# Kernel optimization log

Measured on AMD Instinct MI355X. Metric: run time of the kernel, lower is better.

The kernel has to match this reference:

```python
import jax, jax.numpy as jnp
import numpy as np

B, T, D, R = 8, 4096, 1024, 1024
INIT = 0.02

def setup_inputs() -> dict:
    key = jax.random.key(0)
    ks = jax.random.split(key, 8)
    x = jax.random.normal(ks[0], (B, T, D), dtype=jnp.float32)
    attention_mask = jnp.ones((B, T), dtype=bool)
    W_Q = jax.random.normal(ks[1], (D, D), dtype=jnp.float32) * (1.0 / np.sqrt(D))
    W_K = jax.random.normal(ks[2], (D, D), dtype=jnp.float32) * (1.0 / np.sqrt(D))
    U = jax.random.normal(ks[3], (D, R), dtype=jnp.float32) * INIT
    V = jax.random.normal(ks[4], (D, R), dtype=jnp.float32) * INIT
    Wb = jax.random.normal(ks[5], (D, R), dtype=jnp.float32) * INIT
    bias = jnp.zeros((D,), dtype=jnp.float32)
    W_O = jax.random.normal(ks[6], (D, D), dtype=jnp.float32) * (1.0 / np.sqrt(D))
    return {"x": x, "attention_mask": attention_mask, "W_Q": W_Q, "W_K": W_K,
            "U": U, "V": V, "Wb": Wb, "bias": bias, "W_O": W_O}

def reference(x, attention_mask, W_Q, W_K, U, V, Wb, bias, W_O):
    # Q = x @ W_Q^T, K = x @ W_K^T  (torch Linear stores weight as (out,in))
    Q = jnp.einsum('btd,ed->bte', x, W_Q)
    K = jnp.einsum('btd,ed->bte', x, W_K)
    m = attention_mask.astype(x.dtype)               # (B,T)
    A = Q @ V                                        # (B,T,R)  = Q_i V
    Kw = (K @ Wb) * m[..., None]                     # pad-masked K_j W
    S = jnp.cumsum(Kw, axis=1)                       # causal prefix sum over j<=i
    n = jnp.cumsum(m, axis=1)[..., None]             # n_valid per i, (B,T,1)
    # sum_{j<=i} BCN(Q_i,K_j) = ((Q_iV) * S_i) U^T + n_i * bias; then divide by max(n_i,1)
    out = ((A * S) @ U.T + n * bias) / jnp.clip(n, 1.0)
    return jnp.einsum('btd,ed->bte', out, W_O)
```

## Files before the change

kernel.cpp:

```cpp
#include <hip/hip_runtime.h>
#include <hip/hip_bf16.h>

typedef __attribute__((ext_vector_type(8))) short short8;
typedef __attribute__((ext_vector_type(4))) float f32x4;

#define Bc 8
#define Tc 4096
#define Dc 1024
#define Rc 1024
#define BT (Bc*Tc)

__device__ inline float b2f(ushort u) {
    union { float f; unsigned int i; } x; x.i = ((unsigned int)u) << 16; return x.f;
}
__device__ inline ushort f2b(float f) {
    union { float f; unsigned int i; } x; x.f = f;
    unsigned int r = x.i + 0x7fffu + ((x.i >> 16) & 1u);
    return (ushort)(r >> 16);
}

__device__ inline void gload16(const void* g, void* l) {
    __builtin_amdgcn_global_load_lds(
        (const __attribute__((address_space(1))) unsigned int*)g,
        (__attribute__((address_space(3))) unsigned int*)l, 16, 0, 0);
}


__device__ __attribute__((always_inline)) inline
short8 lds_frag(const char* mat, int rowbase, int k, int fr, int hi) {
    const int row = rowbase + fr;
    const int byte = (row << 7) + (((k << 6) + (hi << 4)) ^ ((row & 7) << 4));
    return *(const short8*)(mat + byte);
}

template<int KK>
__device__ __attribute__((always_inline)) inline
void rdb(const char* BB, short8 (&bf)[2][4], int wn, int fr, int hi) {
#pragma unroll
    for (int n = 0; n < 4; ++n)
        bf[KK][n] = lds_frag(BB, (wn << 6) + (n << 4), KK, fr, hi);
}

template<int MQ, int KK>
__device__ __attribute__((always_inline)) inline
void rda(const char* AB, short8 (&af)[4], int wm, int fr, int hi) {
#pragma unroll
    for (int i = 0; i < 4; ++i)
        af[i] = lds_frag(AB, (wm << 7) + ((MQ * 4 + i) << 4), KK, fr, hi);
}

template<int MQ, int KK>
__device__ __attribute__((always_inline)) inline
void mmq(f32x4 (&acc)[8][4], const short8 (&af)[4], const short8 (&bf)[2][4]) {
#pragma unroll
    for (int i = 0; i < 4; ++i)
#pragma unroll
        for (int n = 0; n < 4; ++n)
            acc[MQ * 4 + i][n] = __builtin_amdgcn_mfma_f32_16x16x32_bf16(
                af[i], bf[KK][n], acc[MQ * 4 + i][n], 0, 0, 0);
}

#define MID do { __builtin_amdgcn_sched_barrier(0); __builtin_amdgcn_s_barrier(); \
    asm volatile("s_waitcnt lgkmcnt(0)" ::: "memory"); __builtin_amdgcn_sched_barrier(0); \
    __builtin_amdgcn_s_setprio(1); } while (0)
#define PEND do { __builtin_amdgcn_s_setprio(0); __builtin_amdgcn_sched_barrier(0); \
    __builtin_amdgcn_s_barrier(); } while (0)
#define PENDVM do { __builtin_amdgcn_s_setprio(0); __builtin_amdgcn_sched_barrier(0); \
    asm volatile("s_waitcnt vmcnt(4)" ::: "memory"); __builtin_amdgcn_s_barrier(); } while (0)

#define STG(G, ld, grow0, gk, lbase) do { \
    const ushort* _s0 = (G) + (size_t)((grow0) + srow) * (ld) + (gk) + scg; \
    const ushort* _s1 = (G) + (size_t)((grow0) + 64 + srow) * (ld) + (gk) + scg; \
    char* _d = (lbase) + (w << 10) + (l << 4); \
    gload16(_s0, _d); gload16(_s1, _d + 8192); } while (0)

template<int EPI>
__global__ __launch_bounds__(512, 2)
void gemm256(const ushort* __restrict__ A, const ushort* __restrict__ Bt,
             void* __restrict__ Cout, const float* __restrict__ bias,
             int ntx, int K, int lda, int ldb, int ldc) {
    __shared__ __align__(16) char sA[65536];
    __shared__ __align__(16) char sB[65536];

    const int tid = threadIdx.x;
    const int w = tid >> 6, l = tid & 63;
    const int wm = w >> 2, wn = w & 3;
    const int fr = l & 15, hi = l >> 4;
    const int srow = (w << 3) + (l >> 3);
    const int scg = (((l & 7) ^ (l >> 3)) << 3);

    const int nwg = (int)gridDim.x;
    const int q = nwg >> 3;
    const int bid = (int)blockIdx.x;
    const int swz = (bid & 7) * q + (bid >> 3);
    const int by = swz / ntx, bx = swz % ntx;
    const int m0 = by << 8, n0 = bx << 8;

    f32x4 acc[8][4] = {};
    short8 af[4], bf[2][4];
    const int NT = K >> 6;

    STG(A,  lda, m0,        0,  sA);
    STG(A,  lda, m0 + 128,  0,  sA + 16384);
    STG(Bt, ldb, n0,        0,  sB);
    STG(Bt, ldb, n0 + 128,  0,  sB + 16384);
    STG(Bt, ldb, n0,        64, sB + 32768);
    STG(Bt, ldb, n0 + 128,  64, sB + 32768 + 16384);
    asm volatile("s_waitcnt vmcnt(4)" ::: "memory");
    __builtin_amdgcn_sched_barrier(0);
    __builtin_amdgcn_s_barrier();

    const char* cA0 = sA;
    const char* cB0 = sB;
    const char* cA1 = sA + 32768;
    const char* cB1 = sB + 32768;

    for (int it = 0; it < (NT >> 1); ++it) {
        const int t1 = 2 * it + 1;
        const int t2 = min(2 * it + 2, NT - 1);
        const int t3 = min(2 * it + 3, NT - 1);

        rdb<0>(cB0, bf, wn, fr, hi); rdb<1>(cB0, bf, wn, fr, hi);
        rda<0, 0>(cA0, af, wm, fr, hi);
        STG(A, lda, m0, t1 << 6, sA + 32768);
        MID; mmq<0, 0>(acc, af, bf); PEND;
        rda<1, 0>(cA0, af, wm, fr, hi);
        STG(A, lda, m0 + 128, t1 << 6, sA + 32768 + 16384);
        MID; mmq<1, 0>(acc, af, bf); PEND;
        rda<0, 1>(cA0, af, wm, fr, hi);
        STG(Bt, ldb, n0, t2 << 6, sB);
        MID; mmq<0, 1>(acc, af, bf); PEND;
        rda<1, 1>(cA0, af, wm, fr, hi);
        STG(Bt, ldb, n0 + 128, t2 << 6, sB + 16384);
        MID; mmq<1, 1>(acc, af, bf); PENDVM;

        rdb<0>(cB1, bf, wn, fr, hi); rdb<1>(cB1, bf, wn, fr, hi);
        rda<0, 0>(cA1, af, wm, fr, hi);
        STG(A, lda, m0, t2 << 6, sA);
        MID; mmq<0, 0>(acc, af, bf); PEND;
        rda<1, 0>(cA1, af, wm, fr, hi);
        STG(A, lda, m0 + 128, t2 << 6, sA + 16384);
        MID; mmq<1, 0>(acc, af, bf); PEND;
        rda<0, 1>(cA1, af, wm, fr, hi);
        STG(Bt, ldb, n0, t3 << 6, sB + 32768);
        MID; mmq<0, 1>(acc, af, bf); PEND;
        rda<1, 1>(cA1, af, wm, fr, hi);
        STG(Bt, ldb, n0 + 128, t3 << 6, sB + 32768 + 16384);
        MID; mmq<1, 1>(acc, af, bf); PENDVM;
    }

    const int crow = m0 + (wm << 7);
    const int ccol = n0 + (wn << 6);
#pragma unroll
    for (int m = 0; m < 8; ++m) {
#pragma unroll
        for (int n = 0; n < 4; ++n) {
            const int r0 = crow + (m << 4) + (hi << 2);
            const int c = ccol + (n << 4) + fr;
            if (EPI == 0) {
                ushort* C = (ushort*)Cout;
#pragma unroll
                for (int t = 0; t < 4; ++t)
                    C[(size_t)(r0 + t) * ldc + c] = f2b(acc[m][n][t]);
            } else {
                float* C = (float*)Cout;
                const float bv = bias[c];
#pragma unroll
                for (int t = 0; t < 4; ++t)
                    C[(size_t)(r0 + t) * ldc + c] = acc[m][n][t] + bv;
            }
        }
    }
}

__global__ void cast_f32_bf16(const float4* __restrict__ in, ushort4* __restrict__ out, int n4) {
    int i = blockIdx.x * blockDim.x + threadIdx.x;
    int stride = gridDim.x * blockDim.x;
    for (; i < n4; i += stride) {
        float4 v = in[i];
        ushort4 o;
        o.x = f2b(v.x); o.y = f2b(v.y); o.z = f2b(v.z); o.w = f2b(v.w);
        out[i] = o;
    }
}

__global__ void transpose_cast(const float* __restrict__ in, ushort* __restrict__ out,
                               int rows, int cols) {
    __shared__ float tile[32][33];
    int c0 = blockIdx.x * 32, r0 = blockIdx.y * 32;
    int tx = threadIdx.x & 31, ty = threadIdx.x >> 5;
    for (int i = 0; i < 32; i += 8)
        tile[ty + i][tx] = in[(size_t)(r0 + ty + i) * cols + c0 + tx];
    __syncthreads();
    for (int i = 0; i < 32; i += 8)
        out[(size_t)(c0 + ty + i) * rows + r0 + tx] = f2b(tile[tx][ty + i]);
}

__global__ __launch_bounds__(256)
void gemm_bt_kernel(const ushort* __restrict__ A, const ushort* __restrict__ Bt,
                    ushort* __restrict__ Cout,
                    int M, int N, int K, int lda, int ldb, int ldc) {
    __shared__ __align__(16) ushort As[128][32];
    __shared__ __align__(16) ushort Bs[128][32];
    const int tid = threadIdx.x;
    const int wave = tid >> 6, lane = tid & 63;
    const int m0 = blockIdx.y * 128, n0 = blockIdx.x * 128;
    const int wr = (wave >> 1) * 64, wc = (wave & 1) * 64;

    f32x4 acc[4][4] = {};

    const int rS = wave * 32 + (lane >> 2);
    const int kS = (lane & 3) * 8;
    const int fr = lane & 15;
    const int fq = (lane >> 4) * 8;

    const int nk = K >> 5;
    for (int kt = 0; kt < nk; ++kt) {
        const int k0 = kt << 5;
        __syncthreads();
        gload16(A  + (size_t)(m0 + rS) * lda      + k0 + kS, &As[rS][kS]);
        gload16(A  + (size_t)(m0 + rS + 16) * lda + k0 + kS, &As[rS + 16][kS]);
        gload16(Bt + (size_t)(n0 + rS) * ldb      + k0 + kS, &Bs[rS][kS]);
        gload16(Bt + (size_t)(n0 + rS + 16) * ldb + k0 + kS, &Bs[rS + 16][kS]);
        __syncthreads();

        short8 af[4], bfr[4];
        #pragma unroll
        for (int i = 0; i < 4; i++) af[i]  = *(const short8*)&As[wr + i * 16 + fr][fq];
        #pragma unroll
        for (int i = 0; i < 4; i++) bfr[i] = *(const short8*)&Bs[wc + i * 16 + fr][fq];
        #pragma unroll
        for (int i = 0; i < 4; i++)
            #pragma unroll
            for (int j = 0; j < 4; j++)
                acc[i][j] = __builtin_amdgcn_mfma_f32_16x16x32_bf16(af[i], bfr[j], acc[i][j], 0, 0, 0);
    }

    const int rq = (lane >> 4) * 4;
    #pragma unroll
    for (int i = 0; i < 4; i++) {
        #pragma unroll
        for (int j = 0; j < 4; j++) {
            int row = m0 + wr + i * 16 + rq;
            int col = n0 + wc + j * 16 + fr;
            #pragma unroll
            for (int t = 0; t < 4; t++)
                Cout[(size_t)(row + t) * ldc + col] = f2b(acc[i][j][t]);
        }
    }
}

__global__ void bias_O_kernel(const float* __restrict__ W_O, const float* __restrict__ bias,
                              float* __restrict__ biasO) {
    __shared__ float sh[256];
    int e = blockIdx.x, tid = threadIdx.x;
    float s = 0.f;
    for (int d = tid; d < Dc; d += 256) s += W_O[(size_t)e * Dc + d] * bias[d];
    sh[tid] = s; __syncthreads();
    for (int o = 128; o > 0; o >>= 1) { if (tid < o) sh[tid] += sh[tid + o]; __syncthreads(); }
    if (tid == 0) biasO[e] = sh[0];
}

__global__ void mask_scan(const int* __restrict__ mask, float* __restrict__ nbuf) {
    __shared__ float sh[256];
    int b = blockIdx.x, tid = threadIdx.x;
    float run = 0.f;
    for (int t0 = 0; t0 < Tc; t0 += 256) {
        float v = (mask[b * Tc + t0 + tid] != 0) ? 1.f : 0.f;
        sh[tid] = v; __syncthreads();
        for (int off = 1; off < 256; off <<= 1) {
            float add = (tid >= off) ? sh[tid - off] : 0.f;
            __syncthreads();
            sh[tid] += add;
            __syncthreads();
        }
        nbuf[b * Tc + t0 + tid] = run + sh[tid];
        run += sh[255];
        __syncthreads();
    }
}

#define NCHUNK 16
#define LCHUNK (Tc / NCHUNK)

__global__ void scan_partial(const ushort* __restrict__ AKw, const int* __restrict__ mask,
                             float* __restrict__ csum) {
    int r = blockIdx.x * 256 + threadIdx.x;
    int chunk = blockIdx.y, b = blockIdx.z;
    int row0 = b * Tc + chunk * LCHUNK;
    const ushort* p = AKw + (size_t)row0 * 2048 + 1024 + r;
    float s = 0.f;
    for (int t = 0; t < LCHUNK; ++t) {
        float mv = (mask[row0 + t] != 0) ? 1.f : 0.f;
        s += mv * b2f(p[(size_t)t * 2048]);
    }
    csum[((size_t)b * NCHUNK + chunk) * Rc + r] = s;
}

__global__ void scan_offsets(float* __restrict__ csum) {
    int r = blockIdx.x * 256 + threadIdx.x;
    int b = blockIdx.y;
    float run = 0.f;
    for (int c = 0; c < NCHUNK; ++c) {
        size_t i = ((size_t)b * NCHUNK + c) * Rc + r;
        float v = csum[i]; csum[i] = run; run += v;
    }
}

__global__ void scan_apply(ushort* __restrict__ AKw, const int* __restrict__ mask,
                           const float* __restrict__ csum, const float* __restrict__ nbuf) {
    int r = blockIdx.x * 256 + threadIdx.x;
    int chunk = blockIdx.y, b = blockIdx.z;
    int row0 = b * Tc + chunk * LCHUNK;
    float s = csum[((size_t)b * NCHUNK + chunk) * Rc + r];
    ushort* p = AKw + (size_t)row0 * 2048;
    for (int t = 0; t < LCHUNK; ++t) {
        size_t off = (size_t)t * 2048;
        float mv = (mask[row0 + t] != 0) ? 1.f : 0.f;
        s += mv * b2f(p[off + 1024 + r]);
        float nv = fmaxf(nbuf[row0 + t], 1.f);
        float pv = b2f(p[off + r]) * s / nv;
        p[off + r] = f2b(pv);
    }
}

extern "C" void kernel_launch(void* const* d_in, const int* in_sizes, int n_in,
                              void* d_out, int out_size, void* d_ws, size_t ws_size,
                              hipStream_t stream) {
    const float* x    = (const float*)d_in[0];
    const int*   mask = (const int*)d_in[1];
    const float* W_Q  = (const float*)d_in[2];
    const float* W_K  = (const float*)d_in[3];
    const float* U    = (const float*)d_in[4];
    const float* V    = (const float*)d_in[5];
    const float* Wb   = (const float*)d_in[6];
    const float* bias = (const float*)d_in[7];
    const float* W_O  = (const float*)d_in[8];
    float* out = (float*)d_out;

    char* ws = (char*)d_ws;
    ushort* xb   = (ushort*)ws; ws += (size_t)BT * Dc * 2;
    ushort* AKw  = (ushort*)ws; ws += (size_t)BT * 2048 * 2;
    ushort* W1   = (ushort*)ws; ws += (size_t)2048 * Dc * 2;
    ushort* Mmat = (ushort*)ws; ws += (size_t)Dc * Rc * 2;
    ushort* Vt   = (ushort*)ws; ws += (size_t)Dc * Rc * 2;
    ushort* Wbt  = (ushort*)ws; ws += (size_t)Dc * Rc * 2;
    ushort* Ut   = (ushort*)ws; ws += (size_t)Dc * Rc * 2;
    ushort* WQt  = (ushort*)ws; ws += (size_t)Dc * Dc * 2;
    ushort* WKt  = (ushort*)ws; ws += (size_t)Dc * Dc * 2;
    ushort* WOb  = (ushort*)ws; ws += (size_t)Dc * Dc * 2;
    float*  csum = (float*)ws;  ws += (size_t)Bc * NCHUNK * Rc * 4;
    float*  nbuf = (float*)ws;  ws += (size_t)Bc * Tc * 4;
    float*  biasO = (float*)ws; ws += (size_t)Dc * 4;

    cast_f32_bf16<<<2048, 256, 0, stream>>>((const float4*)x, (ushort4*)xb, BT * Dc / 4);
    cast_f32_bf16<<<256, 256, 0, stream>>>((const float4*)W_O, (ushort4*)WOb, Dc * Dc / 4);

    transpose_cast<<<dim3(32, 32), 256, 0, stream>>>(V,   Vt,  Dc, Rc);
    transpose_cast<<<dim3(32, 32), 256, 0, stream>>>(Wb,  Wbt, Dc, Rc);
    transpose_cast<<<dim3(32, 32), 256, 0, stream>>>(U,   Ut,  Dc, Rc);
    transpose_cast<<<dim3(32, 32), 256, 0, stream>>>(W_Q, WQt, Dc, Dc);
    transpose_cast<<<dim3(32, 32), 256, 0, stream>>>(W_K, WKt, Dc, Dc);

    gemm_bt_kernel<<<dim3(8, 8), 256, 0, stream>>>(Vt,  WQt, W1,                   Rc, Dc, Dc, Dc, Dc, Dc);
    gemm_bt_kernel<<<dim3(8, 8), 256, 0, stream>>>(Wbt, WKt, W1 + (size_t)Rc * Dc, Rc, Dc, Dc, Dc, Dc, Dc);
    gemm_bt_kernel<<<dim3(8, 8), 256, 0, stream>>>(WOb, Ut,  Mmat,                 Dc, Rc, Dc, Dc, Dc, Rc);
    bias_O_kernel<<<Dc, 256, 0, stream>>>(W_O, bias, biasO);

    gemm256<0><<<1024, 512, 0, stream>>>(xb, W1, AKw, nullptr, 8, Dc, Dc, Dc, 2048);

    mask_scan<<<Bc, 256, 0, stream>>>(mask, nbuf);
    scan_partial<<<dim3(4, NCHUNK, Bc), 256, 0, stream>>>(AKw, mask, csum);
    scan_offsets<<<dim3(4, Bc), 256, 0, stream>>>(csum);
    scan_apply<<<dim3(4, NCHUNK, Bc), 256, 0, stream>>>(AKw, mask, csum, nbuf);

    gemm256<1><<<512, 512, 0, stream>>>(AKw, Mmat, out, biasO, 4, Rc, 2048, Rc, Dc);
}
```

Measured before the change: 452.7 us.

## Restructure GEMM pipeline, batch weight prep kernels, vectorize chunked scan

Reworks the main GEMM inner loop so each 64-wide K step double-buffers A fragments, drops the per-phase lgkmcnt(0) wait, and precomputes per-thread global and LDS offsets. Merges the five transpose-casts plus the W_O cast into one launch, and the three small weight GEMMs into one z-batched launch. Rewrites the scan kernels to use 64 chunks, have each thread handle four columns with vector loads, skip masked rows, and multiply by a reciprocal instead of dividing. Removing the lgkmcnt wait leans on the compiler to insert its own LDS waits, and the extra fragment registers could hurt occupancy.

```diff
diff --git a/kernel.cpp b/kernel.cpp
--- a/kernel.cpp
+++ b/kernel.cpp
@@ -60,19 +60,38 @@
                 af[i], bf[KK][n], acc[MQ * 4 + i][n], 0, 0, 0);
 }
 
-#define MID do { __builtin_amdgcn_sched_barrier(0); __builtin_amdgcn_s_barrier(); \
-    asm volatile("s_waitcnt lgkmcnt(0)" ::: "memory"); __builtin_amdgcn_sched_barrier(0); \
+#define PH_MID do { __builtin_amdgcn_sched_barrier(0); __builtin_amdgcn_s_barrier(); \
     __builtin_amdgcn_s_setprio(1); } while (0)
-#define PEND do { __builtin_amdgcn_s_setprio(0); __builtin_amdgcn_sched_barrier(0); \
+#define PH_END do { __builtin_amdgcn_s_setprio(0); __builtin_amdgcn_sched_barrier(0); \
     __builtin_amdgcn_s_barrier(); } while (0)
-#define PENDVM do { __builtin_amdgcn_s_setprio(0); __builtin_amdgcn_sched_barrier(0); \
-    asm volatile("s_waitcnt vmcnt(4)" ::: "memory"); __builtin_amdgcn_s_barrier(); } while (0)
-
-#define STG(G, ld, grow0, gk, lbase) do { \
-    const ushort* _s0 = (G) + (size_t)((grow0) + srow) * (ld) + (gk) + scg; \
-    const ushort* _s1 = (G) + (size_t)((grow0) + 64 + srow) * (ld) + (gk) + scg; \
-    char* _d = (lbase) + (w << 10) + (l << 4); \
-    gload16(_s0, _d); gload16(_s1, _d + 8192); } while (0)
+
+#define STG(G, ld, thr, grow0, gk, lbase) do { \
+    const ushort* _p = (G) + (size_t)(grow0) * (ld) + (gk); \
+    gload16(_p + (thr), (lbase) + thrD); \
+    gload16(_p + (size_t)64 * (ld) + (thr), (lbase) + thrD + 8192); } while (0)
+
+#define TILE(cAb, cBb, stA, stB, tn, tn2) do { \
+     \
+    rdb<0>(cBb, bf, wn, fr, hi); \
+    rda<0, 0>(cAb, afA, wm, fr, hi); \
+    rda<1, 0>(cAb, afB, wm, fr, hi); \
+    STG(A, lda, thrA, m0, (tn) << 6, stA); \
+    PH_MID; mmq<0, 0>(acc, afA, bf); PH_END; \
+     \
+    rdb<1>(cBb, bf, wn, fr, hi); \
+    rda<0, 1>(cAb, afA, wm, fr, hi); \
+    STG(A, lda, thrA, m0 + 128, (tn) << 6, stA + 16384); \
+    PH_MID; mmq<1, 0>(acc, afB, bf); PH_END; \
+     \
+    rda<1, 1>(cAb, afB, wm, fr, hi); \
+    PH_MID; mmq<0, 1>(acc, afA, bf); PH_END; \
+     \
+    STG(Bt, ldb, thrB, n0,       (tn2) << 6, stB); \
+    STG(Bt, ldb, thrB, n0 + 128, (tn2) << 6, stB + 16384); \
+    PH_MID; mmq<1, 1>(acc, afB, bf); \
+    __builtin_amdgcn_s_setprio(0); __builtin_amdgcn_sched_barrier(0); \
+    asm volatile("s_waitcnt vmcnt(4)" ::: "memory"); \
+    __builtin_amdgcn_s_barrier(); } while (0)
 
 template<int EPI>
 __global__ __launch_bounds__(512, 2)
@@ -88,6 +107,9 @@
     const int fr = l & 15, hi = l >> 4;
     const int srow = (w << 3) + (l >> 3);
     const int scg = (((l & 7) ^ (l >> 3)) << 3);
+    const size_t thrA = (size_t)srow * lda + scg;
+    const size_t thrB = (size_t)srow * ldb + scg;
+    const int thrD = (w << 10) + (l << 4);
 
     const int nwg = (int)gridDim.x;
     const int q = nwg >> 3;
@@ -97,15 +119,15 @@
     const int m0 = by << 8, n0 = bx << 8;
 
     f32x4 acc[8][4] = {};
-    short8 af[4], bf[2][4];
+    short8 afA[4], afB[4], bf[2][4];
     const int NT = K >> 6;
 
-    STG(A,  lda, m0,        0,  sA);
-    STG(A,  lda, m0 + 128,  0,  sA + 16384);
-    STG(Bt, ldb, n0,        0,  sB);
-    STG(Bt, ldb, n0 + 128,  0,  sB + 16384);
-    STG(Bt, ldb, n0,        64, sB + 32768);
-    STG(Bt, ldb, n0 + 128,  64, sB + 32768 + 16384);
+    STG(A,  lda, thrA, m0,        0,  sA);
+    STG(A,  lda, thrA, m0 + 128,  0,  sA + 16384);
+    STG(Bt, ldb, thrB, n0,        0,  sB);
+    STG(Bt, ldb, thrB, n0 + 128,  0,  sB + 16384);
+    STG(Bt, ldb, thrB, n0,        64, sB + 32768);
+    STG(Bt, ldb, thrB, n0 + 128,  64, sB + 32768 + 16384);
     asm volatile("s_waitcnt vmcnt(4)" ::: "memory");
     __builtin_amdgcn_sched_barrier(0);
     __builtin_amdgcn_s_barrier();
@@ -119,34 +141,8 @@
         const int t1 = 2 * it + 1;
         const int t2 = min(2 * it + 2, NT - 1);
         const int t3 = min(2 * it + 3, NT - 1);
-
-        rdb<0>(cB0, bf, wn, fr, hi); rdb<1>(cB0, bf, wn, fr, hi);
-        rda<0, 0>(cA0, af, wm, fr, hi);
-        STG(A, lda, m0, t1 << 6, sA + 32768);
-        MID; mmq<0, 0>(acc, af, bf); PEND;
-        rda<1, 0>(cA0, af, wm, fr, hi);
-        STG(A, lda, m0 + 128, t1 << 6, sA + 32768 + 16384);
-        MID; mmq<1, 0>(acc, af, bf); PEND;
-        rda<0, 1>(cA0, af, wm, fr, hi);
-        STG(Bt, ldb, n0, t2 << 6, sB);
-        MID; mmq<0, 1>(acc, af, bf); PEND;
-        rda<1, 1>(cA0, af, wm, fr, hi);
-        STG(Bt, ldb, n0 + 128, t2 << 6, sB + 16384);
-        MID; mmq<1, 1>(acc, af, bf); PENDVM;
-
-        rdb<0>(cB1, bf, wn, fr, hi); rdb<1>(cB1, bf, wn, fr, hi);
-        rda<0, 0>(cA1, af, wm, fr, hi);
-        STG(A, lda, m0, t2 << 6, sA);
-        MID; mmq<0, 0>(acc, af, bf); PEND;
-        rda<1, 0>(cA1, af, wm, fr, hi);
-        STG(A, lda, m0 + 128, t2 << 6, sA + 16384);
-        MID; mmq<1, 0>(acc, af, bf); PEND;
-        rda<0, 1>(cA1, af, wm, fr, hi);
-        STG(Bt, ldb, n0, t3 << 6, sB + 32768);
-        MID; mmq<0, 1>(acc, af, bf); PEND;
-        rda<1, 1>(cA1, af, wm, fr, hi);
-        STG(Bt, ldb, n0 + 128, t3 << 6, sB + 32768 + 16384);
-        MID; mmq<1, 1>(acc, af, bf); PENDVM;
+        TILE(cA0, cB0, sA + 32768, sB, t1, t2);
+        TILE(cA1, cB1, sA, sB + 32768, t2, t3);
     }
 
     const int crow = m0 + (wm << 7);
@@ -184,22 +180,48 @@
     }
 }
 
-__global__ void transpose_cast(const float* __restrict__ in, ushort* __restrict__ out,
-                               int rows, int cols) {
+__global__ void prep_weights(const float* __restrict__ V,  const float* __restrict__ Wb,
+                             const float* __restrict__ U,  const float* __restrict__ WQ,
+                             const float* __restrict__ WK, const float* __restrict__ WO,
+                             ushort* __restrict__ Vt,  ushort* __restrict__ Wbt,
+                             ushort* __restrict__ Ut,  ushort* __restrict__ WQt,
+                             ushort* __restrict__ WKt, ushort* __restrict__ WOb) {
     __shared__ float tile[32][33];
+    const float* in; ushort* out;
+    switch (blockIdx.z) {
+        case 0: in = V;  out = Vt;  break;
+        case 1: in = Wb; out = Wbt; break;
+        case 2: in = U;  out = Ut;  break;
+        case 3: in = WQ; out = WQt; break;
+        case 4: in = WK; out = WKt; break;
+        default: in = WO; out = WOb; break;
+    }
     int c0 = blockIdx.x * 32, r0 = blockIdx.y * 32;
     int tx = threadIdx.x & 31, ty = threadIdx.x >> 5;
-    for (int i = 0; i < 32; i += 8)
-        tile[ty + i][tx] = in[(size_t)(r0 + ty + i) * cols + c0 + tx];
-    __syncthreads();
-    for (int i = 0; i < 32; i += 8)
-        out[(size_t)(c0 + ty + i) * rows + r0 + tx] = f2b(tile[tx][ty + i]);
+    if (blockIdx.z < 5) {
+        for (int i = 0; i < 32; i += 8)
+            tile[ty + i][tx] = in[(size_t)(r0 + ty + i) * 1024 + c0 + tx];
+        __syncthreads();
+        for (int i = 0; i < 32; i += 8)
+            out[(size_t)(c0 + ty + i) * 1024 + r0 + tx] = f2b(tile[tx][ty + i]);
+    } else {
+        for (int i = 0; i < 32; i += 8)
+            out[(size_t)(r0 + ty + i) * 1024 + c0 + tx] =
+                f2b(in[(size_t)(r0 + ty + i) * 1024 + c0 + tx]);
+    }
 }
 
 __global__ __launch_bounds__(256)
-void gemm_bt_kernel(const ushort* __restrict__ A, const ushort* __restrict__ Bt,
-                    ushort* __restrict__ Cout,
-                    int M, int N, int K, int lda, int ldb, int ldc) {
+void gemm_bt3(const ushort* __restrict__ Vt,  const ushort* __restrict__ WQt,
+              const ushort* __restrict__ Wbt, const ushort* __restrict__ WKt,
+              const ushort* __restrict__ WOb, const ushort* __restrict__ Ut,
+              ushort* __restrict__ W1, ushort* __restrict__ Mmat) {
+    const ushort *A, *Bt; ushort* Cout;
+    switch (blockIdx.z) {
+        case 0: A = Vt;  Bt = WQt; Cout = W1; break;
+        case 1: A = Wbt; Bt = WKt; Cout = W1 + (size_t)Rc * Dc; break;
+        default: A = WOb; Bt = Ut; Cout = Mmat; break;
+    }
     __shared__ __align__(16) ushort As[128][32];
     __shared__ __align__(16) ushort Bs[128][32];
     const int tid = threadIdx.x;
@@ -214,14 +236,13 @@
     const int fr = lane & 15;
     const int fq = (lane >> 4) * 8;
 
-    const int nk = K >> 5;
-    for (int kt = 0; kt < nk; ++kt) {
+    for (int kt = 0; kt < 32; ++kt) {
         const int k0 = kt << 5;
         __syncthreads();
-        gload16(A  + (size_t)(m0 + rS) * lda      + k0 + kS, &As[rS][kS]);
-        gload16(A  + (size_t)(m0 + rS + 16) * lda + k0 + kS, &As[rS + 16][kS]);
-        gload16(Bt + (size_t)(n0 + rS) * ldb      + k0 + kS, &Bs[rS][kS]);
-        gload16(Bt + (size_t)(n0 + rS + 16) * ldb + k0 + kS, &Bs[rS + 16][kS]);
+        gload16(A  + (size_t)(m0 + rS) * 1024      + k0 + kS, &As[rS][kS]);
+        gload16(A  + (size_t)(m0 + rS + 16) * 1024 + k0 + kS, &As[rS + 16][kS]);
+        gload16(Bt + (size_t)(n0 + rS) * 1024      + k0 + kS, &Bs[rS][kS]);
+        gload16(Bt + (size_t)(n0 + rS + 16) * 1024 + k0 + kS, &Bs[rS + 16][kS]);
         __syncthreads();
 
         short8 af[4], bfr[4];
@@ -245,7 +266,7 @@
             int col = n0 + wc + j * 16 + fr;
             #pragma unroll
             for (int t = 0; t < 4; t++)
-                Cout[(size_t)(row + t) * ldc + col] = f2b(acc[i][j][t]);
+                Cout[(size_t)(row + t) * 1024 + col] = f2b(acc[i][j][t]);
         }
     }
 }
@@ -280,47 +301,57 @@
     }
 }
 
-#define NCHUNK 16
+#define NCHUNK 64
 #define LCHUNK (Tc / NCHUNK)
 
 __global__ void scan_partial(const ushort* __restrict__ AKw, const int* __restrict__ mask,
                              float* __restrict__ csum) {
-    int r = blockIdx.x * 256 + threadIdx.x;
-    int chunk = blockIdx.y, b = blockIdx.z;
-    int row0 = b * Tc + chunk * LCHUNK;
+    const int r = threadIdx.x * 4;
+    const int chunk = blockIdx.x, b = blockIdx.y;
+    const int row0 = b * Tc + chunk * LCHUNK;
     const ushort* p = AKw + (size_t)row0 * 2048 + 1024 + r;
-    float s = 0.f;
+    float4 s = {0.f, 0.f, 0.f, 0.f};
     for (int t = 0; t < LCHUNK; ++t) {
-        float mv = (mask[row0 + t] != 0) ? 1.f : 0.f;
-        s += mv * b2f(p[(size_t)t * 2048]);
-    }
-    csum[((size_t)b * NCHUNK + chunk) * Rc + r] = s;
+        if (mask[row0 + t] != 0) {
+            ushort4 q = *(const ushort4*)(p + (size_t)t * 2048);
+            s.x += b2f(q.x); s.y += b2f(q.y); s.z += b2f(q.z); s.w += b2f(q.w);
+        }
+    }
+    *(float4*)(csum + (((size_t)b * NCHUNK + chunk) << 10) + r) = s;
 }
 
 __global__ void scan_offsets(float* __restrict__ csum) {
-    int r = blockIdx.x * 256 + threadIdx.x;
-    int b = blockIdx.y;
-    float run = 0.f;
+    const int r = threadIdx.x * 4;
+    const int b = blockIdx.x;
+    float4 run = {0.f, 0.f, 0.f, 0.f};
     for (int c = 0; c < NCHUNK; ++c) {
-        size_t i = ((size_t)b * NCHUNK + c) * Rc + r;
-        float v = csum[i]; csum[i] = run; run += v;
+        float4* p = (float4*)(csum + (((size_t)b * NCHUNK + c) << 10) + r);
+        float4 v = *p; *p = run;
+        run.x += v.x; run.y += v.y; run.z += v.z; run.w += v.w;
     }
 }
 
 __global__ void scan_apply(ushort* __restrict__ AKw, const int* __restrict__ mask,
                            const float* __restrict__ csum, const float* __restrict__ nbuf) {
-    int r = blockIdx.x * 256 + threadIdx.x;
-    int chunk = blockIdx.y, b = blockIdx.z;
-    int row0 = b * Tc + chunk * LCHUNK;
-    float s = csum[((size_t)b * NCHUNK + chunk) * Rc + r];
-    ushort* p = AKw + (size_t)row0 * 2048;
+    const int r = threadIdx.x * 4;
+    const int chunk = blockIdx.x, b = blockIdx.y;
+    const int row0 = b * Tc + chunk * LCHUNK;
+    float4 s = *(const float4*)(csum + (((size_t)b * NCHUNK + chunk) << 10) + r);
+    ushort* p = AKw + (size_t)row0 * 2048 + r;
     for (int t = 0; t < LCHUNK; ++t) {
-        size_t off = (size_t)t * 2048;
-        float mv = (mask[row0 + t] != 0) ? 1.f : 0.f;
-        s += mv * b2f(p[off + 1024 + r]);
-        float nv = fmaxf(nbuf[row0 + t], 1.f);
-        float pv = b2f(p[off + r]) * s / nv;
-        p[off + r] = f2b(pv);
+        const size_t off = (size_t)t * 2048;
+        if (mask[row0 + t] != 0) {
+            ushort4 kw = *(const ushort4*)(p + off + 1024);
+            s.x += b2f(kw.x); s.y += b2f(kw.y); s.z += b2f(kw.z); s.w += b2f(kw.w);
+        }
+        const float rn = 1.f / fmaxf(nbuf[row0 + t], 1.f);
+        ushort4 a = *(const ushort4*)(p + off);
+        ushort4 o;
+        o.x = f2b(b2f(a.x) * s.x * rn);
+        o.y = f2b(b2f(a.y) * s.y * rn);
+        o.z = f2b(b2f(a.z) * s.z * rn);
+        o.w = f2b(b2f(a.w) * s.w * rn);
+        *(ushort4*)(p + off) = o;
     }
 }
 
@@ -354,25 +385,18 @@
     float*  biasO = (float*)ws; ws += (size_t)Dc * 4;
 
     cast_f32_bf16<<<2048, 256, 0, stream>>>((const float4*)x, (ushort4*)xb, BT * Dc / 4);
-    cast_f32_bf16<<<256, 256, 0, stream>>>((const float4*)W_O, (ushort4*)WOb, Dc * Dc / 4);
-
-    transpose_cast<<<dim3(32, 32), 256, 0, stream>>>(V,   Vt,  Dc, Rc);
-    transpose_cast<<<dim3(32, 32), 256, 0, stream>>>(Wb,  Wbt, Dc, Rc);
-    transpose_cast<<<dim3(32, 32), 256, 0, stream>>>(U,   Ut,  Dc, Rc);
-    transpose_cast<<<dim3(32, 32), 256, 0, stream>>>(W_Q, WQt, Dc, Dc);
-    transpose_cast<<<dim3(32, 32), 256, 0, stream>>>(W_K, WKt, Dc, Dc);
-
-    gemm_bt_kernel<<<dim3(8, 8), 256, 0, stream>>>(Vt,  WQt, W1,                   Rc, Dc, Dc, Dc, Dc, Dc);
-    gemm_bt_kernel<<<dim3(8, 8), 256, 0, stream>>>(Wbt, WKt, W1 + (size_t)Rc * Dc, Rc, Dc, Dc, Dc, Dc, Dc);
-    gemm_bt_kernel<<<dim3(8, 8), 256, 0, stream>>>(WOb, Ut,  Mmat,                 Dc, Rc, Dc, Dc, Dc, Rc);
+    prep_weights<<<dim3(32, 32, 6), 256, 0, stream>>>(V, Wb, U, W_Q, W_K, W_O,
+                                                      Vt, Wbt, Ut, WQt, WKt, WOb);
+
+    gemm_bt3<<<dim3(8, 8, 3), 256, 0, stream>>>(Vt, WQt, Wbt, WKt, WOb, Ut, W1, Mmat);
     bias_O_kernel<<<Dc, 256, 0, stream>>>(W_O, bias, biasO);
 
     gemm256<0><<<1024, 512, 0, stream>>>(xb, W1, AKw, nullptr, 8, Dc, Dc, Dc, 2048);
 
     mask_scan<<<Bc, 256, 0, stream>>>(mask, nbuf);
-    scan_partial<<<dim3(4, NCHUNK, Bc), 256, 0, stream>>>(AKw, mask, csum);
-    scan_offsets<<<dim3(4, Bc), 256, 0, stream>>>(csum);
-    scan_apply<<<dim3(4, NCHUNK, Bc), 256, 0, stream>>>(AKw, mask, csum, nbuf);
+    scan_partial<<<dim3(NCHUNK, Bc), 256, 0, stream>>>(AKw, mask, csum);
+    scan_offsets<<<Bc, 256, 0, stream>>>(csum);
+    scan_apply<<<dim3(NCHUNK, Bc), 256, 0, stream>>>(AKw, mask, csum, nbuf);
 
     gemm256<1><<<512, 512, 0, stream>>>(AKw, Mmat, out, biasO, 4, Rc, 2048, Rc, Dc);
 }
```

After: 406.5 us. 10.2% less time.
